# Kernel tuning notes

Hardware: AMD Instinct MI355X
Metric: run time of the kernel (lower is better)

Reference implementation:

```python
import jax, jax.numpy as jnp
import numpy as np

ENT_TOTAL = 100000
REL_TOTAL = 1000
ENT_SIZE = 200
REL_SIZE = 200
BATCH = 16384
MARGIN = 4.0


def setup_inputs() -> dict:
    key = jax.random.key(0)
    ks = jax.random.split(key, 8)
    return {
        "pos_h": jax.random.randint(ks[0], (BATCH,), 0, ENT_TOTAL, dtype=jnp.int32),
        "pos_t": jax.random.randint(ks[1], (BATCH,), 0, ENT_TOTAL, dtype=jnp.int32),
        "pos_r": jax.random.randint(ks[2], (BATCH,), 0, REL_TOTAL, dtype=jnp.int32),
        "neg_h": jax.random.randint(ks[3], (BATCH,), 0, ENT_TOTAL, dtype=jnp.int32),
        "neg_t": jax.random.randint(ks[4], (BATCH,), 0, ENT_TOTAL, dtype=jnp.int32),
        "ent_emb": jax.random.normal(ks[5], (ENT_TOTAL, ENT_SIZE), dtype=jnp.float32) * 0.1,
        "rel_emb": jax.random.normal(ks[6], (REL_TOTAL, REL_SIZE), dtype=jnp.float32) * 0.1,
        "transfer": jax.random.normal(ks[7], (REL_TOTAL, ENT_SIZE * REL_SIZE), dtype=jnp.float32) * 0.05,
    }


def _l2norm(x):
    # tf.nn.l2_normalize semantics: x / sqrt(max(sum(x^2), eps))
    return x * jax.lax.rsqrt(jnp.maximum(jnp.sum(x * x, axis=-1, keepdims=True), 1e-12))


def _calc(h, t, r):
    return jnp.abs(_l2norm(h) + _l2norm(r) - _l2norm(t))


def reference(pos_h, pos_t, pos_r, neg_h, neg_t, ent_emb, rel_emb, transfer):
    # gather embeddings
    pos_h_e = ent_emb[pos_h]                 # [b, ent]
    pos_t_e = ent_emb[pos_t]
    pos_r_e = rel_emb[pos_r]                 # [b, rel]
    neg_h_e = ent_emb[neg_h]
    neg_t_e = ent_emb[neg_t]
    # relation-specific transfer matrices [b, ent, rel]
    pos_mat = transfer[pos_r].reshape(-1, ENT_SIZE, REL_SIZE)
    # project entities into relation space: [b, ent] x [b, ent, rel] -> [b, rel]
    p_h = jnp.einsum('be,ber->br', pos_h_e, pos_mat)
    p_t = jnp.einsum('be,ber->br', pos_t_e, pos_mat)
    n_h = jnp.einsum('be,ber->br', neg_h_e, pos_mat)  # negative_rel == 0: reuse pos matrix
    n_t = jnp.einsum('be,ber->br', neg_t_e, pos_mat)
    p_score = jnp.sum(_calc(p_h, p_t, pos_r_e), axis=-1, keepdims=True)  # [b,1]
    n_score = jnp.sum(_calc(n_h, n_t, pos_r_e), axis=-1, keepdims=True)
    loss = jnp.mean(jnp.maximum(p_score - n_score + MARGIN, 0.0))
    return loss
```

## Files before the change

### kernel.cpp

```cpp
#include <hip/hip_runtime.h>

#define ENT 200
#define RELD 200
#define NREL 1000
#define NBATCH 16384
#define MARGIN 4.0f
#define CHUNK 16
#define NVEC 64
#define MAXCHUNKS 2048

#define BSTRIDE_I 211
#define BBUF 844

#define WS_COUNTS 0
#define WS_CURSORS 1024
#define WS_OFFSETS 2048
#define WS_NCHUNKS 3072
#define WS_CHUNKS 3076
#define WS_LIST 11268
#define WS_ELEM 27652

typedef __attribute__((ext_vector_type(8))) short short8;
typedef __attribute__((ext_vector_type(4))) float floatx4;

__device__ __forceinline__ unsigned short f2bf(float x) {
    unsigned u = __float_as_uint(x);
    u = (u + 0x7FFFu + ((u >> 16) & 1u)) >> 16;
    return (unsigned short)u;
}

__device__ __forceinline__ float wave_reduce(float v) {
#pragma unroll
    for (int off = 32; off > 0; off >>= 1) v += __shfl_down(v, off, 64);
    return v;
}

__global__ __launch_bounds__(1024) void zero_kernel(int* ws) {
    for (int i = threadIdx.x; i < 3076; i += 1024) ws[i] = 0;
}

__global__ __launch_bounds__(256) void count_kernel(const int* __restrict__ pos_r, int* ws) {
    const int i = blockIdx.x * 256 + threadIdx.x;
    if (i < NBATCH) atomicAdd(&ws[WS_COUNTS + pos_r[i]], 1);
}

__global__ __launch_bounds__(1024) void scan_kernel(int* ws) {
    __shared__ int s[1024];
    const int tid = threadIdx.x;
    const int cnt = (tid < NREL) ? ws[WS_COUNTS + tid] : 0;
    s[tid] = cnt;
    __syncthreads();
#pragma unroll
    for (int off = 1; off < 1024; off <<= 1) {
        const int add = (tid >= off) ? s[tid - off] : 0;
        __syncthreads();
        s[tid] += add;
        __syncthreads();
    }
    const int myoff = s[tid] - cnt;
    if (tid < NREL) ws[WS_OFFSETS + tid] = myoff;
    __syncthreads();
    const int nch = (cnt + CHUNK - 1) / CHUNK;
    s[tid] = nch;
    __syncthreads();
#pragma unroll
    for (int off = 1; off < 1024; off <<= 1) {
        const int add = (tid >= off) ? s[tid - off] : 0;
        __syncthreads();
        s[tid] += add;
        __syncthreads();
    }
    const int cbase = s[tid] - nch;
    int4* chunks = (int4*)(ws + WS_CHUNKS);
    for (int k = 0; k < nch; ++k)
        chunks[cbase + k] = make_int4(tid, myoff + CHUNK * k, min(CHUNK, cnt - CHUNK * k), 0);
    if (tid == 1023) ws[WS_NCHUNKS] = s[1023];
}

__global__ __launch_bounds__(256) void fill_kernel(const int* __restrict__ pos_r, int* ws) {
    const int i = blockIdx.x * 256 + threadIdx.x;
    if (i < NBATCH) {
        const int r = pos_r[i];
        const int p = ws[WS_OFFSETS + r] + atomicAdd(&ws[WS_CURSORS + r], 1);
        ws[WS_LIST + p] = i;
    }
}

__global__ __launch_bounds__(256) void transr_mfma_kernel(
    const int* __restrict__ pos_h, const int* __restrict__ pos_t,
    const int* __restrict__ neg_h, const int* __restrict__ neg_t,
    const float* __restrict__ ent_emb, const float* __restrict__ rel_emb,
    const float* __restrict__ transfer, int* __restrict__ ws)
{
    const int nch = ws[WS_NCHUNKS];
    const int stride = (nch + 7) >> 3;
    const int bidx = blockIdx.x;
    if ((bidx >> 3) >= stride) return;
    const int cix = (bidx & 7) * stride + (bidx >> 3);
    if (cix >= nch) return;

    __shared__ short sB[2 * BBUF * 8];
    __shared__ int items_s[CHUNK];
    __shared__ int rows[NVEC];

    const int4 ck = ((const int4*)(ws + WS_CHUNKS))[cix];
    const int r = ck.x, start = ck.y, cnt = ck.z;

    const int tid  = threadIdx.x;
    const int lane = tid & 63;
    const int wv   = tid >> 6;
    const int q    = lane >> 4;
    const int n    = lane & 15;
    const bool wactive = (wv * 4 < cnt);

    if (tid < CHUNK) items_s[tid] = ws[WS_LIST + start + min(tid, cnt - 1)];
    __syncthreads();
    if (tid < NVEC) {
        const int b = items_s[tid >> 2];
        const int c = tid & 3;
        rows[tid] = (c == 0) ? pos_h[b] : (c == 1) ? pos_t[b] : (c == 2) ? neg_h[b] : neg_t[b];
    }
    __syncthreads();

    short8 afrag[7];
#pragma unroll
    for (int s = 0; s < 7; ++s) afrag[s] = (short8){0, 0, 0, 0, 0, 0, 0, 0};
    if (wactive) {
        const int row = rows[wv * 16 + n];
        const float* __restrict__ ab = ent_emb + (size_t)row * ENT;
#pragma unroll
        for (int s = 0; s < 7; ++s) {
            const int e0 = s * 32 + q * 8;
            if (e0 < ENT) {
                float v[8];
                *(float4*)(&v[0]) = *(const float4*)(ab + e0);
                *(float4*)(&v[4]) = *(const float4*)(ab + e0 + 4);
                short8 f;
#pragma unroll
                for (int j = 0; j < 8; ++j) f[j] = (short)f2bf(v[j]);
                afrag[s] = f;
            }
        }
    }

    const int slot = tid;
    const int sq   = slot / 52;
    const int srem = slot - sq * 52;
    const int scol = srem * 4;
    const bool sact = (slot < 208) && (scol < RELD);
    const float* __restrict__ Mb = transfer + (size_t)r * (ENT * RELD) + scol;
    const int k0 = sq * 8;

    float fm[8][4];
    short8 bh[4];
#define LOAD_SLAB(s_)                                                          \
    {                                                                          \
        const int kk = (s_) * 32 + k0;                                         \
        if (sact && kk < ENT) {                                                \
            _Pragma("unroll")                                                  \
            for (int j = 0; j < 8; ++j)                                        \
                *(float4*)(&fm[j][0]) = *(const float4*)(Mb + (size_t)(kk + j) * RELD); \
        } else {                                                               \
            _Pragma("unroll")                                                  \
            for (int j = 0; j < 8; ++j) {                                      \
                fm[j][0] = 0.f; fm[j][1] = 0.f; fm[j][2] = 0.f; fm[j][3] = 0.f;\
            }                                                                  \
        }                                                                      \
    }
#define CONV_SLAB()                                                            \
    {                                                                          \
        _Pragma("unroll")                                                      \
        for (int i = 0; i < 4; ++i) {                                          \
            short8 f;                                                          \
            _Pragma("unroll")                                                  \
            for (int j = 0; j < 8; ++j) f[j] = (short)f2bf(fm[j][i]);          \
            bh[i] = f;                                                         \
        }                                                                      \
    }
#define WRITE_SLAB(buf_)                                                       \
    if (slot < 208) {                                                          \
        _Pragma("unroll")                                                      \
        for (int i = 0; i < 4; ++i)                                            \
            *(short8*)(&sB[((buf_) * BBUF + i * BSTRIDE_I + slot) * 8]) = bh[i]; \
    }

    floatx4 acc[13];
#pragma unroll
    for (int c = 0; c < 13; ++c) acc[c] = (floatx4){0.f, 0.f, 0.f, 0.f};

    const int rb16 = (n & 3) * BSTRIDE_I + q * 52 + (n >> 2);

    LOAD_SLAB(0); CONV_SLAB(); WRITE_SLAB(0);
    LOAD_SLAB(1); CONV_SLAB();
    __syncthreads();

#pragma unroll
    for (int s = 0; s < 7; ++s) {
        if (s < 5) LOAD_SLAB(s + 2);
        if (wactive) {
            const int bb = (s & 1) * BBUF;
#pragma unroll
            for (int c = 0; c < 13; ++c) {
                const short8 bf = *(const short8*)(&sB[(bb + rb16 + c * 4) * 8]);
                acc[c] = __builtin_amdgcn_mfma_f32_16x16x32_bf16(afrag[s], bf, acc[c], 0, 0, 0);
            }
        }
        if (s < 6) WRITE_SLAB((s + 1) & 1);
        if (s < 5) CONV_SLAB();
        if (s < 6) __syncthreads();
    }

    if (wactive) {
        float rl[13];
        const float* __restrict__ rb = rel_emb + (size_t)r * RELD;
#pragma unroll
        for (int c = 0; c < 13; ++c) {
            const int col = c * 16 + n;
            rl[c] = (col < RELD) ? rb[col] : 0.f;
        }
        float nsq[4] = {0.f, 0.f, 0.f, 0.f};
        float rsq = 0.f;
#pragma unroll
        for (int c = 0; c < 13; ++c) {
            nsq[0] += acc[c][0] * acc[c][0];
            nsq[1] += acc[c][1] * acc[c][1];
            nsq[2] += acc[c][2] * acc[c][2];
            nsq[3] += acc[c][3] * acc[c][3];
            rsq += rl[c] * rl[c];
        }
#pragma unroll
        for (int m = 1; m < 16; m <<= 1) {
#pragma unroll
            for (int k = 0; k < 4; ++k) nsq[k] += __shfl_xor(nsq[k], m, 64);
            rsq += __shfl_xor(rsq, m, 64);
        }
        float inv[4];
#pragma unroll
        for (int k = 0; k < 4; ++k) inv[k] = rsqrtf(fmaxf(nsq[k], 1e-12f));
        const float invr = rsqrtf(fmaxf(rsq, 1e-12f));

        float psum = 0.f, nsum = 0.f;
#pragma unroll
        for (int c = 0; c < 13; ++c) {
            const float rr = rl[c] * invr;
            psum += fabsf(acc[c][0] * inv[0] + rr - acc[c][1] * inv[1]);
            nsum += fabsf(acc[c][2] * inv[2] + rr - acc[c][3] * inv[3]);
        }
#pragma unroll
        for (int m = 1; m < 16; m <<= 1) {
            psum += __shfl_xor(psum, m, 64);
            nsum += __shfl_xor(nsum, m, 64);
        }
        const int item = wv * 4 + q;
        if (n == 0 && item < cnt) {
            float* elem = (float*)(ws + WS_ELEM);
            elem[items_s[item]] = fmaxf(psum - nsum + MARGIN, 0.f);
        }
    }
}

__global__ __launch_bounds__(256) void reduce_mean_kernel(const int* __restrict__ ws,
                                                          float* __restrict__ out) {
    __shared__ float sred[4];
    const float4* elem = (const float4*)(ws + WS_ELEM);
    float s = 0.f;
    for (int i = threadIdx.x; i < NBATCH / 4; i += 256) {
        const float4 v = elem[i];
        s += v.x + v.y + v.z + v.w;
    }
    s = wave_reduce(s);
    const int lane = threadIdx.x & 63;
    const int wvv = threadIdx.x >> 6;
    if (lane == 0) sred[wvv] = s;
    __syncthreads();
    if (threadIdx.x == 0)
        out[0] = (sred[0] + sred[1] + sred[2] + sred[3]) * (1.0f / (float)NBATCH);
}

extern "C" void kernel_launch(void* const* d_in, const int* in_sizes, int n_in,
                              void* d_out, int out_size, void* d_ws, size_t ws_size,
                              hipStream_t stream) {
    const int* pos_h = (const int*)d_in[0];
    const int* pos_t = (const int*)d_in[1];
    const int* pos_r = (const int*)d_in[2];
    const int* neg_h = (const int*)d_in[3];
    const int* neg_t = (const int*)d_in[4];
    const float* ent_emb = (const float*)d_in[5];
    const float* rel_emb = (const float*)d_in[6];
    const float* transfer = (const float*)d_in[7];

    int* ws = (int*)d_ws;
    float* out = (float*)d_out;

    zero_kernel<<<1, 1024, 0, stream>>>(ws);
    count_kernel<<<NBATCH / 256, 256, 0, stream>>>(pos_r, ws);
    scan_kernel<<<1, 1024, 0, stream>>>(ws);
    fill_kernel<<<NBATCH / 256, 256, 0, stream>>>(pos_r, ws);
    transr_mfma_kernel<<<MAXCHUNKS, 256, 0, stream>>>(
        pos_h, pos_t, neg_h, neg_t, ent_emb, rel_emb, transfer, ws);
    reduce_mean_kernel<<<1, 256, 0, stream>>>(ws, out);
}
```

Measured before the change: 310.9 us.

## Fuse bucketing prep into one kernel and enlarge chunks with 512-thread blocks

Replaces the zero, count, scan and fill kernels with a single-block prep kernel that counts, scans and fills the per-relation item lists using shared-memory atomics. This removes several kernel launches and global atomics. The main kernel now processes chunks of up to 32 items with 512-thread blocks, which changes grid size and per-block work. Larger chunks may leave many blocks half-filled, since the average number of items per relation is small.

Result: slower. 473.3 us (+52.2%).

```diff
diff --git a/kernel.cpp b/kernel.cpp
--- a/kernel.cpp
+++ b/kernel.cpp
@@ -5,16 +5,13 @@
 #define NREL 1000
 #define NBATCH 16384
 #define MARGIN 4.0f
-#define CHUNK 16
-#define NVEC 64
-#define MAXCHUNKS 2048
+#define CHUNK 32
+#define NVEC 128
+#define MAXCHUNKS 1512
 
 #define BSTRIDE_I 211
 #define BBUF 844
 
-#define WS_COUNTS 0
-#define WS_CURSORS 1024
-#define WS_OFFSETS 2048
 #define WS_NCHUNKS 3072
 #define WS_CHUNKS 3076
 #define WS_LIST 11268
@@ -35,58 +32,66 @@
     return v;
 }
 
-__global__ __launch_bounds__(1024) void zero_kernel(int* ws) {
-    for (int i = threadIdx.x; i < 3076; i += 1024) ws[i] = 0;
-}
-
-__global__ __launch_bounds__(256) void count_kernel(const int* __restrict__ pos_r, int* ws) {
-    const int i = blockIdx.x * 256 + threadIdx.x;
-    if (i < NBATCH) atomicAdd(&ws[WS_COUNTS + pos_r[i]], 1);
-}
-
-__global__ __launch_bounds__(1024) void scan_kernel(int* ws) {
-    __shared__ int s[1024];
+__global__ __launch_bounds__(1024) void prep_kernel(const int* __restrict__ pos_r,
+                                                    int* __restrict__ ws) {
+    __shared__ int cnt_s[NREL];
+    __shared__ int off_s[NREL];
+    __shared__ int scan_s[1024];
     const int tid = threadIdx.x;
-    const int cnt = (tid < NREL) ? ws[WS_COUNTS + tid] : 0;
-    s[tid] = cnt;
+
+    for (int i = tid; i < NREL; i += 1024) cnt_s[i] = 0;
+    __syncthreads();
+
+    int rl[16];
+#pragma unroll
+    for (int k = 0; k < 16; ++k) {
+        rl[k] = pos_r[(k << 10) + tid];
+        atomicAdd(&cnt_s[rl[k]], 1);
+    }
+    __syncthreads();
+
+    const int cnt = (tid < NREL) ? cnt_s[tid] : 0;
+
+    scan_s[tid] = cnt;
     __syncthreads();
 #pragma unroll
     for (int off = 1; off < 1024; off <<= 1) {
-        const int add = (tid >= off) ? s[tid - off] : 0;
+        const int add = (tid >= off) ? scan_s[tid - off] : 0;
         __syncthreads();
-        s[tid] += add;
+        scan_s[tid] += add;
         __syncthreads();
     }
-    const int myoff = s[tid] - cnt;
-    if (tid < NREL) ws[WS_OFFSETS + tid] = myoff;
-    __syncthreads();
+    const int myoff = scan_s[tid] - cnt;
+    if (tid < NREL) off_s[tid] = myoff;
+    __syncthreads();
+
     const int nch = (cnt + CHUNK - 1) / CHUNK;
-    s[tid] = nch;
+    scan_s[tid] = nch;
     __syncthreads();
 #pragma unroll
     for (int off = 1; off < 1024; off <<= 1) {
-        const int add = (tid >= off) ? s[tid - off] : 0;
+        const int add = (tid >= off) ? scan_s[tid - off] : 0;
         __syncthreads();
-        s[tid] += add;
+        scan_s[tid] += add;
         __syncthreads();
     }
-    const int cbase = s[tid] - nch;
+    const int cbase = scan_s[tid] - nch;
     int4* chunks = (int4*)(ws + WS_CHUNKS);
     for (int k = 0; k < nch; ++k)
         chunks[cbase + k] = make_int4(tid, myoff + CHUNK * k, min(CHUNK, cnt - CHUNK * k), 0);
-    if (tid == 1023) ws[WS_NCHUNKS] = s[1023];
-}
-
-__global__ __launch_bounds__(256) void fill_kernel(const int* __restrict__ pos_r, int* ws) {
-    const int i = blockIdx.x * 256 + threadIdx.x;
-    if (i < NBATCH) {
-        const int r = pos_r[i];
-        const int p = ws[WS_OFFSETS + r] + atomicAdd(&ws[WS_CURSORS + r], 1);
-        ws[WS_LIST + p] = i;
-    }
-}
-
-__global__ __launch_bounds__(256) void transr_mfma_kernel(
+    if (tid == 1023) ws[WS_NCHUNKS] = scan_s[1023];
+
+    if (tid < NREL) cnt_s[tid] = 0;
+    __syncthreads();
+#pragma unroll
+    for (int k = 0; k < 16; ++k) {
+        const int r = rl[k];
+        const int p = off_s[r] + atomicAdd(&cnt_s[r], 1);
+        ws[WS_LIST + p] = (k << 10) + tid;
+    }
+}
+
+__global__ __launch_bounds__(512, 6) void transr_mfma_kernel(
     const int* __restrict__ pos_h, const int* __restrict__ pos_t,
     const int* __restrict__ neg_h, const int* __restrict__ neg_t,
     const float* __restrict__ ent_emb, const float* __restrict__ rel_emb,
@@ -292,11 +297,8 @@
     int* ws = (int*)d_ws;
     float* out = (float*)d_out;
 
-    zero_kernel<<<1, 1024, 0, stream>>>(ws);
-    count_kernel<<<NBATCH / 256, 256, 0, stream>>>(pos_r, ws);
-    scan_kernel<<<1, 1024, 0, stream>>>(ws);
-    fill_kernel<<<NBATCH / 256, 256, 0, stream>>>(pos_r, ws);
-    transr_mfma_kernel<<<MAXCHUNKS, 256, 0, stream>>>(
+    prep_kernel<<<1, 1024, 0, stream>>>(pos_r, ws);
+    transr_mfma_kernel<<<MAXCHUNKS, 512, 0, stream>>>(
         pos_h, pos_t, neg_h, neg_t, ent_emb, rel_emb, transfer, ws);
     reduce_mean_kernel<<<1, 256, 0, stream>>>(ws, out);
 }
```
